# Optimization experiments

Measured on AMD Instinct MI355X. Metric: run time of the kernel, lower is better.

The kernel has to match this reference:

```python
import jax, jax.numpy as jnp
import numpy as np

N = 50000   # nodes
E = 640000  # edges
G = 128     # graphs in batch
H = 128     # hidden_channels
F_NODE, F_EDGE, F_LIG, F_POC = 64, 16, 200, 100
N_STACK = 3  # num_layers - 1


def setup_inputs() -> dict:
    key = jax.random.key(0)
    ks = jax.random.split(key, 24)
    r = lambda i, shape, s=0.05: jax.random.normal(ks[i], shape, dtype=jnp.float32) * s
    z = lambda shape: jnp.zeros(shape, jnp.float32)
    return {
        "x": jax.random.normal(ks[0], (N, F_NODE), dtype=jnp.float32),
        "edge_index": jax.random.randint(ks[1], (2, E), 0, N),
        "edge_attr": jax.random.normal(ks[2], (E, F_EDGE), dtype=jnp.float32),
        "batch": jnp.sort(jax.random.randint(ks[3], (N,), 0, G)),
        "ligand_features": jax.random.normal(ks[4], (G, F_LIG), dtype=jnp.float32),
        "pocket_features": jax.random.normal(ks[5], (G, F_POC), dtype=jnp.float32),
        # conv1 (in != out -> lin_self is a Linear)
        "W1_msg": r(6, (F_NODE, H)), "b1_msg": z((H,)),
        "W1_edge": r(7, (F_EDGE, H)), "b1_edge": z((H,)),
        "W1_self": r(8, (F_NODE, H)), "b1_self": z((H,)),
        # stacked convs (in == out -> lin_self is Identity)
        "Wk_msg": r(9, (N_STACK, H, H)), "bk_msg": z((N_STACK, H)),
        "Wk_edge": r(10, (N_STACK, F_EDGE, H)), "bk_edge": z((N_STACK, H)),
        # global feature / fusion / output heads
        "Wl": r(11, (F_LIG, H)), "bl": z((H,)),
        "Wp": r(12, (F_POC, H)), "bp": z((H,)),
        "Wf": r(13, (3 * H, H)), "bf": z((H,)),
        "Wo": r(14, (H, 1)), "bo": z((1,)),
        "return_embeddings": 0,
    }


def _general_conv(x, edge_index, edge_attr, W_msg, b_msg, W_edge, b_edge, self_out):
    # PyG GeneralConv: msg = lin_msg(x_src) + lin_edge(edge_attr), sum-aggregated at dst,
    # then + lin_self(x) (Identity skip when passed self_out = x).
    src, dst = edge_index[0], edge_index[1]
    edge_term = edge_attr @ W_edge + b_edge            # [E, H] (per-edge, layer-specific)
    msg = x[src] @ W_msg + b_msg + edge_term           # [E, H] gather + GEMM
    agg = jax.ops.segment_sum(msg, dst, num_segments=x.shape[0])  # scatter-add
    return agg + self_out


def reference(x, edge_index, edge_attr, batch, ligand_features, pocket_features,
              W1_msg, b1_msg, W1_edge, b1_edge, W1_self, b1_self,
              Wk_msg, bk_msg, Wk_edge, bk_edge,
              Wl, bl, Wp, bp, Wf, bf, Wo, bo, return_embeddings):
    # conv1 with linear self-connection
    h = _general_conv(x, edge_index, edge_attr, W1_msg, b1_msg, W1_edge, b1_edge,
                      x @ W1_self + b1_self)
    h = jax.nn.relu(h)
    # stacked convs with identity self-connection
    for i in range(N_STACK):
        h = _general_conv(h, edge_index, edge_attr, Wk_msg[i], bk_msg[i],
                          Wk_edge[i], bk_edge[i], h)
        h = jax.nn.relu(h)
    # global mean pool over graphs
    sums = jax.ops.segment_sum(h, batch, num_segments=G)
    counts = jax.ops.segment_sum(jnp.ones((h.shape[0],), h.dtype), batch, num_segments=G)
    pooled = sums / jnp.maximum(counts, 1.0)[:, None]
    # global feature fusion
    lig = ligand_features @ Wl + bl
    poc = pocket_features @ Wp + bp
    fused = jnp.concatenate([pooled, lig, poc], axis=1) @ Wf + bf
    # dropout is a no-op in eval mode
    if not return_embeddings:
        fused = fused @ Wo + bo
    return fused
```

## Files before the change

kernel.cpp:

```cpp
#include <hip/hip_runtime.h>
#include <cstdint>

#define NN 50000
#define NE 640000
#define NG 128
#define HD 128
#define FN 64
#define FE 16
#define FL 200
#define FPOC 100
#define NSTACK 3
#define NBUK 196

typedef unsigned short ushort_t;
typedef short short8 __attribute__((ext_vector_type(8)));
typedef float f32x4 __attribute__((ext_vector_type(4)));

__device__ __forceinline__ ushort_t f2bf(float f) {
    unsigned u = __float_as_uint(f);
    unsigned r = (u + 0x7fffu + ((u >> 16) & 1u)) >> 16;
    return (ushort_t)r;
}
__device__ __forceinline__ float bf2f(ushort_t u) {
    return __uint_as_float(((unsigned)u) << 16);
}


__global__ void hist_kernel(const int* __restrict__ ei, int* __restrict__ bucket_cnt) {
    __shared__ int l[NBUK];
    int t = threadIdx.x;
    if (t < NBUK) l[t] = 0;
    __syncthreads();
    int base = blockIdx.x * 2048;
#pragma unroll
    for (int i = 0; i < 8; ++i) {
        int e = base + i * 256 + t;
        if (e < NE) atomicAdd(&l[ei[NE + e] >> 8], 1);
    }
    __syncthreads();
    if (t < NBUK && l[t]) atomicAdd(&bucket_cnt[t], l[t]);
}

__global__ void scan_kernel(const int* __restrict__ bucket_cnt,
                            int* __restrict__ bucket_base, int* __restrict__ bucket_cur) {
    __shared__ int s[256];
    int t = threadIdx.x;
    int v = (t < NBUK) ? bucket_cnt[t] : 0;
    s[t] = v;
    __syncthreads();
    for (int off = 1; off < 256; off <<= 1) {
        int w = (t >= off) ? s[t - off] : 0;
        __syncthreads();
        s[t] += w;
        __syncthreads();
    }
    if (t < NBUK) {
        int b = s[t] - v;
        bucket_base[t] = b;
        bucket_cur[t] = b;
    }
}

__global__ __launch_bounds__(256) void scatter_bin(const int* __restrict__ ei,
                                                   int* __restrict__ bucket_cur,
                                                   int2* __restrict__ staging) {
    __shared__ int lcnt[NBUK];
    __shared__ int lrun[NBUK];
    int t = threadIdx.x;
    if (t < NBUK) lcnt[t] = 0;
    __syncthreads();
    int base = blockIdx.x * 4096;
#pragma unroll
    for (int i = 0; i < 16; ++i) {
        int e = base + i * 256 + t;
        if (e < NE) atomicAdd(&lcnt[ei[NE + e] >> 8], 1);
    }
    __syncthreads();
    if (t < NBUK) {
        int c = lcnt[t];
        lrun[t] = c ? atomicAdd(&bucket_cur[t], c) : 0;
        lcnt[t] = 0;
    }
    __syncthreads();
#pragma unroll
    for (int i = 0; i < 16; ++i) {
        int e = base + i * 256 + t;
        if (e < NE) {
            int s = ei[e];
            int d = ei[NE + e];
            int bk = d >> 8;
            int off = atomicAdd(&lcnt[bk], 1);
            staging[lrun[bk] + off] = make_int2(s, e | ((d & 255) << 20));
        }
    }
}

__global__ __launch_bounds__(256) void place_kernel(
    const int* __restrict__ bucket_base, const int* __restrict__ bucket_cnt,
    const int2* __restrict__ staging, int* __restrict__ row_beg,
    int* __restrict__ csrc, int* __restrict__ cedge) {
    __shared__ int hist[256];
    __shared__ int curp[256];
    int t = threadIdx.x;
    int b = blockIdx.x;
    int n0 = b << 8;
    hist[t] = 0;
    __syncthreads();
    int ebase = bucket_base[b];
    int ecnt = bucket_cnt[b];
    for (int i = t; i < ecnt; i += 256) atomicAdd(&hist[staging[ebase + i].y >> 20], 1);
    __syncthreads();
    int v = hist[t];
    __syncthreads();
    for (int off = 1; off < 256; off <<= 1) {
        int w = (t >= off) ? hist[t - off] : 0;
        __syncthreads();
        hist[t] += w;
        __syncthreads();
    }
    int rb = ebase + hist[t] - v;
    if (n0 + t < NN) row_beg[n0 + t] = rb;
    if (b == 0 && t == 0) row_beg[NN] = NE;
    curp[t] = rb;
    __syncthreads();
    for (int i = t; i < ecnt; i += 256) {
        int2 p = staging[ebase + i];
        int dl = p.y >> 20;
        int e = p.y & 0xFFFFF;
        int pos = atomicAdd(&curp[dl], 1);
        csrc[pos] = p.x;
        cedge[pos] = e;
    }
}

__global__ __launch_bounds__(256) void sege_kernel(
    const int* __restrict__ row_beg, const int* __restrict__ cedge,
    const float* __restrict__ ea, ushort_t* __restrict__ segaug) {
    int node = blockIdx.x * 4 + (threadIdx.x >> 6);
    if (node >= NN) return;
    int lane = threadIdx.x & 63;
    int G = lane >> 2, q4 = (lane & 3) * 4;
    int beg = row_beg[node], end = row_beg[node + 1];
    int dg = end - beg;
    float4 a = make_float4(0.f, 0.f, 0.f, 0.f);
    for (int j = beg + G; j < end; j += 16) {
        int e = cedge[j];
        float4 v = *(const float4*)(ea + (size_t)e * FE + q4);
        a.x += v.x; a.y += v.y; a.z += v.z; a.w += v.w;
    }
    for (int m = 4; m <= 32; m <<= 1) {
        a.x += __shfl_xor(a.x, m);
        a.y += __shfl_xor(a.y, m);
        a.z += __shfl_xor(a.z, m);
        a.w += __shfl_xor(a.w, m);
    }
    if (lane < 4) {
        ushort_t o[4] = {f2bf(a.x), f2bf(a.y), f2bf(a.z), f2bf(a.w)};
        *(uint2*)(segaug + (size_t)node * 32 + lane * 4) = *(uint2*)o;
    } else if (lane < 8) {
        ushort_t o[4] = {0, 0, 0, 0};
        if (lane == 4) { o[0] = f2bf((float)dg); o[1] = f2bf(1.f); }
        *(uint2*)(segaug + (size_t)node * 32 + lane * 4) = *(uint2*)o;
    }
}


__global__ void repack_kernel(const float* __restrict__ W1_msg,
                              const float* __restrict__ W1_self,
                              const float* __restrict__ W1_edge,
                              const float* __restrict__ b1_msg,
                              const float* __restrict__ b1_edge,
                              const float* __restrict__ b1_self,
                              const float* __restrict__ Wk_msg,
                              const float* __restrict__ Wk_edge,
                              const float* __restrict__ bk_msg,
                              const float* __restrict__ bk_edge,
                              ushort_t* __restrict__ pack) {
    int mid = blockIdx.y;
    const float *W = nullptr, *bm = nullptr, *be = nullptr, *bc = nullptr;
    int K;
    size_t doff;
    bool aug = false;
    if (mid == 0)      { W = W1_msg;  K = 64;  doff = 0; }
    else if (mid == 1) { W = W1_self; K = 64;  doff = 8192; }
    else if (mid == 2) { W = W1_edge; bm = b1_msg; be = b1_edge; bc = b1_self;
                         K = 32; doff = 16384; aug = true; }
    else if (mid <= 5) { int i = mid - 3; W = Wk_msg + (size_t)i * HD * HD;
                         K = 128; doff = 20480 + (size_t)i * 16384; }
    else               { int i = mid - 6; W = Wk_edge + (size_t)i * FE * HD;
                         bm = bk_msg + i * HD; be = bk_edge + i * HD;
                         K = 32; doff = 69632 + (size_t)i * 4096; aug = true; }
    int KS = K / 32;
    int t = blockIdx.x * 256 + threadIdx.x;
    if (t >= 8 * KS * 64) return;
    int lane = t & 63;
    int nk = t >> 6;
    int ks = nk % KS, nt = nk / KS;
    int n = nt * 16 + (lane & 15);
    int kb = ks * 32 + (lane >> 4) * 8;
    ushort_t o[8];
#pragma unroll
    for (int j = 0; j < 8; ++j) {
        int k = kb + j;
        float v;
        if (!aug)         v = W[(size_t)k * HD + n];
        else if (k < 16)  v = W[(size_t)k * HD + n];
        else if (k == 16) v = bm[n] + be[n];
        else if (k == 17) v = bc ? bc[n] : 0.f;
        else              v = 0.f;
        o[j] = f2bf(v);
    }
    *(uint4*)(pack + doff + (size_t)t * 8) = *(uint4*)o;
}


__global__ __launch_bounds__(256) void gemm_mfma_conv1(const float* __restrict__ A,
                                                       const ushort_t* __restrict__ segaug,
                                                       const ushort_t* __restrict__ pack,
                                                       ushort_t* __restrict__ Cm,
                                                       ushort_t* __restrict__ Cs, int n) {
    constexpr int STR = 72, SSTR = 40;
    __shared__ __align__(16) ushort_t As[64 * STR];
    __shared__ __align__(16) ushort_t Ss[64 * SSTR];
    int tid = threadIdx.x;
    int row0 = blockIdx.x * 64;
#pragma unroll
    for (int p = 0; p < 2; ++p) {
        int c = p * 256 + tid;
        int r = c >> 3, col = (c & 7) * 8;
        int gr = row0 + r;
        float4 f0 = make_float4(0.f, 0.f, 0.f, 0.f), f1 = f0;
        if (gr < n) {
            f0 = *(const float4*)(A + (size_t)gr * FN + col);
            f1 = *(const float4*)(A + (size_t)gr * FN + col + 4);
        }
        ushort_t o[8] = {f2bf(f0.x), f2bf(f0.y), f2bf(f0.z), f2bf(f0.w),
                         f2bf(f1.x), f2bf(f1.y), f2bf(f1.z), f2bf(f1.w)};
        *(uint4*)(&As[r * STR + col]) = *(uint4*)o;
    }
    {
        int c = tid;
        int r = c >> 2, col = (c & 3) * 8;
        int gr = row0 + r;
        uint4 v = make_uint4(0u, 0u, 0u, 0u);
        if (gr < n) v = *(const uint4*)(segaug + (size_t)gr * 32 + col);
        *(uint4*)(&Ss[r * SSTR + col]) = v;
    }
    __syncthreads();
    int lane = tid & 63, wave = tid >> 6;
    int m = lane & 15, quad = lane >> 4;
    f32x4 acc[16];
#pragma unroll
    for (int i = 0; i < 16; ++i) acc[i] = (f32x4)(0.f);
    const short8* Bmsg = (const short8*)pack;
    const short8* Bself = (const short8*)(pack + 8192);
    const short8* Beaug = (const short8*)(pack + 16384);
#pragma unroll
    for (int ks = 0; ks < 2; ++ks) {
        short8 a = *(const short8*)(&As[(wave * 16 + m) * STR + ks * 32 + quad * 8]);
#pragma unroll
        for (int nt = 0; nt < 8; ++nt) {
            acc[nt] = __builtin_amdgcn_mfma_f32_16x16x32_bf16(
                a, Bmsg[(nt * 2 + ks) * 64 + lane], acc[nt], 0, 0, 0);
            acc[8 + nt] = __builtin_amdgcn_mfma_f32_16x16x32_bf16(
                a, Bself[(nt * 2 + ks) * 64 + lane], acc[8 + nt], 0, 0, 0);
        }
    }
    {
        short8 sa = *(const short8*)(&Ss[(wave * 16 + m) * SSTR + quad * 8]);
#pragma unroll
        for (int nt = 0; nt < 8; ++nt)
            acc[8 + nt] = __builtin_amdgcn_mfma_f32_16x16x32_bf16(
                sa, Beaug[nt * 64 + lane], acc[8 + nt], 0, 0, 0);
    }
#pragma unroll
    for (int nt = 0; nt < 8; ++nt) {
        int col = nt * 16 + m;
#pragma unroll
        for (int r = 0; r < 4; ++r) {
            int grow = row0 + wave * 16 + quad * 4 + r;
            if (grow < n) {
                Cm[(size_t)grow * HD + col] = f2bf(acc[nt][r]);
                Cs[(size_t)grow * HD + col] = f2bf(acc[8 + nt][r]);
            }
        }
    }
}


__device__ __forceinline__ void accum8(float* a, uint4 v) {
    a[0] += __uint_as_float(v.x << 16);
    a[1] += __uint_as_float(v.x & 0xffff0000u);
    a[2] += __uint_as_float(v.y << 16);
    a[3] += __uint_as_float(v.y & 0xffff0000u);
    a[4] += __uint_as_float(v.z << 16);
    a[5] += __uint_as_float(v.z & 0xffff0000u);
    a[6] += __uint_as_float(v.w << 16);
    a[7] += __uint_as_float(v.w & 0xffff0000u);
}

#define AGG_LOOP(SRCBUF)                                                       \
    {                                                                          \
        int j = beg;                                                           \
        for (; j + 3 < end; j += 4) {                                          \
            int u0 = csrc[j], u1 = csrc[j + 1], u2 = csrc[j + 2],              \
                u3 = csrc[j + 3];                                              \
            uint4 v0 = *(const uint4*)(SRCBUF + (size_t)u0 * HD + c8);         \
            uint4 v1 = *(const uint4*)(SRCBUF + (size_t)u1 * HD + c8);         \
            uint4 v2 = *(const uint4*)(SRCBUF + (size_t)u2 * HD + c8);         \
            uint4 v3 = *(const uint4*)(SRCBUF + (size_t)u3 * HD + c8);         \
            accum8(a0, v0);                                                    \
            accum8(a1, v1);                                                    \
            accum8(a0, v2);                                                    \
            accum8(a1, v3);                                                    \
        }                                                                      \
        for (; j < end; ++j) {                                                 \
            uint4 v = *(const uint4*)(SRCBUF + (size_t)csrc[j] * HD + c8);     \
            accum8(a0, v);                                                     \
        }                                                                      \
    }

__global__ __launch_bounds__(256, 6) void fused_agg_gemm(
    const int* __restrict__ row_beg, const int* __restrict__ csrc,
    const ushort_t* __restrict__ msg_in, const ushort_t* __restrict__ S_in,
    const ushort_t* __restrict__ segaug, const ushort_t* __restrict__ Bm,
    const ushort_t* __restrict__ Be, ushort_t* __restrict__ msg_out,
    ushort_t* __restrict__ S_out) {
    constexpr int STR = 136, SSTR = 40;
    __shared__ __align__(16) ushort_t Hs[16 * STR];
    __shared__ __align__(16) ushort_t Ss[16 * SSTR];
    int tid = threadIdx.x;
    int node0 = blockIdx.x * 16;
    if (tid < 64) {
        int r = tid >> 2, col = (tid & 3) * 8;
        *(uint4*)(&Ss[r * SSTR + col]) =
            *(const uint4*)(segaug + (size_t)(node0 + r) * 32 + col);
    }
    int nl = tid >> 4;
    int node = node0 + nl;
    int c8 = (tid & 15) * 8;
    int beg = row_beg[node];
    int end = row_beg[node + 1];
    float a0[8] = {0.f, 0.f, 0.f, 0.f, 0.f, 0.f, 0.f, 0.f};
    float a1[8] = {0.f, 0.f, 0.f, 0.f, 0.f, 0.f, 0.f, 0.f};
    AGG_LOOP(msg_in)
    accum8(a0, *(const uint4*)(S_in + (size_t)node * HD + c8));
    {
        ushort_t h8[8];
#pragma unroll
        for (int i = 0; i < 8; ++i) h8[i] = f2bf(fmaxf(a0[i] + a1[i], 0.f));
        *(uint4*)(&Hs[nl * STR + c8]) = *(uint4*)h8;
    }
    __syncthreads();
    int lane = tid & 63, wave = tid >> 6;
    int m = lane & 15, quad = lane >> 4;
    f32x4 acc[2], accE[2];
#pragma unroll
    for (int t = 0; t < 2; ++t) { acc[t] = (f32x4)(0.f); accE[t] = (f32x4)(0.f); }
    const short8* Bmv = (const short8*)Bm;
    const short8* Bev = (const short8*)Be;
#pragma unroll
    for (int ks = 0; ks < 4; ++ks) {
        short8 a = *(const short8*)(&Hs[m * STR + ks * 32 + quad * 8]);
#pragma unroll
        for (int t = 0; t < 2; ++t) {
            int nt = wave * 2 + t;
            acc[t] = __builtin_amdgcn_mfma_f32_16x16x32_bf16(
                a, Bmv[(nt * 4 + ks) * 64 + lane], acc[t], 0, 0, 0);
        }
    }
    {
        short8 sa = *(const short8*)(&Ss[m * SSTR + quad * 8]);
#pragma unroll
        for (int t = 0; t < 2; ++t) {
            int nt = wave * 2 + t;
            accE[t] = __builtin_amdgcn_mfma_f32_16x16x32_bf16(
                sa, Bev[nt * 64 + lane], accE[t], 0, 0, 0);
        }
    }
#pragma unroll
    for (int t = 0; t < 2; ++t) {
        int col = (wave * 2 + t) * 16 + m;
#pragma unroll
        for (int r = 0; r < 4; ++r) {
            int rl = quad * 4 + r;
            size_t gidx = (size_t)(node0 + rl) * HD + col;
            msg_out[gidx] = f2bf(acc[t][r]);
            S_out[gidx] = f2bf(accE[t][r] + bf2f(Hs[rl * STR + col]));
        }
    }
}


__global__ __launch_bounds__(256, 6) void agg_pool_kernel(
    const int* __restrict__ row_beg, const int* __restrict__ csrc,
    const ushort_t* __restrict__ xm, const ushort_t* __restrict__ selfb,
    const int* __restrict__ batch, float* __restrict__ pooled) {
    __shared__ float hloc[16][HD];
    int tid = threadIdx.x;
    int node0 = blockIdx.x * 16;
    int nl = tid >> 4;
    int node = node0 + nl;
    int c8 = (tid & 15) * 8;
    int beg = row_beg[node];
    int end = row_beg[node + 1];
    float a0[8] = {0.f, 0.f, 0.f, 0.f, 0.f, 0.f, 0.f, 0.f};
    float a1[8] = {0.f, 0.f, 0.f, 0.f, 0.f, 0.f, 0.f, 0.f};
    AGG_LOOP(xm)
    accum8(a0, *(const uint4*)(selfb + (size_t)node * HD + c8));
#pragma unroll
    for (int i = 0; i < 8; ++i) hloc[nl][c8 + i] = fmaxf(a0[i] + a1[i], 0.f);
    __syncthreads();
    if (tid < HD) {
        int f = tid;
        float run = 0.f;
        int gprev = batch[node0];
        for (int r = 0; r < 16; ++r) {
            int g = batch[node0 + r];
            if (g != gprev) {
                atomicAdd(&pooled[gprev * HD + f], run);
                run = 0.f;
                gprev = g;
            }
            run += hloc[r][f];
        }
        atomicAdd(&pooled[gprev * HD + f], run);
    }
}


__global__ void head_kernel(const float* __restrict__ pooled, const int* __restrict__ batch,
                            const float* __restrict__ lf, const float* __restrict__ pfe,
                            const float* __restrict__ Wl, const float* __restrict__ bl,
                            const float* __restrict__ Wp, const float* __restrict__ bp,
                            const float* __restrict__ Wf, const float* __restrict__ bfv,
                            const float* __restrict__ Wo, const float* __restrict__ bo,
                            float* __restrict__ out) {
    __shared__ float cat[3 * HD];
    __shared__ float red[HD];
    int g = blockIdx.x, j = threadIdx.x;
    int lo = 0, hi = NN;
    while (lo < hi) { int m = (lo + hi) >> 1; if (batch[m] < g) lo = m + 1; else hi = m; }
    int s0 = lo;
    lo = s0; hi = NN;
    while (lo < hi) { int m = (lo + hi) >> 1; if (batch[m] < g + 1) lo = m + 1; else hi = m; }
    float cntf = (float)(lo - s0);
    cat[j] = pooled[(size_t)g * HD + j] / fmaxf(cntf, 1.f);
    float s = bl[j];
    for (int k = 0; k < FL; ++k) s += lf[g * FL + k] * Wl[k * HD + j];
    cat[HD + j] = s;
    s = bp[j];
    for (int k = 0; k < FPOC; ++k) s += pfe[g * FPOC + k] * Wp[k * HD + j];
    cat[2 * HD + j] = s;
    __syncthreads();
    float fj = bfv[j];
    for (int k = 0; k < 3 * HD; ++k) fj += cat[k] * Wf[k * HD + j];
    red[j] = fj * Wo[j];
    __syncthreads();
    for (int off = 64; off > 0; off >>= 1) {
        if (j < off) red[j] += red[j + off];
        __syncthreads();
    }
    if (j == 0) out[g] = red[0] + bo[0];
}


extern "C" void kernel_launch(void* const* d_in, const int* in_sizes, int n_in,
                              void* d_out, int out_size, void* d_ws, size_t ws_size,
                              hipStream_t stream) {
    const float* x       = (const float*)d_in[0];
    const int*   ei      = (const int*)d_in[1];
    const float* ea      = (const float*)d_in[2];
    const int*   batch   = (const int*)d_in[3];
    const float* lf      = (const float*)d_in[4];
    const float* pfe     = (const float*)d_in[5];
    const float* W1_msg  = (const float*)d_in[6];
    const float* b1_msg  = (const float*)d_in[7];
    const float* W1_edge = (const float*)d_in[8];
    const float* b1_edge = (const float*)d_in[9];
    const float* W1_self = (const float*)d_in[10];
    const float* b1_self = (const float*)d_in[11];
    const float* Wk_msg  = (const float*)d_in[12];
    const float* bk_msg  = (const float*)d_in[13];
    const float* Wk_edge = (const float*)d_in[14];
    const float* bk_edge = (const float*)d_in[15];
    const float* Wl      = (const float*)d_in[16];
    const float* bl      = (const float*)d_in[17];
    const float* Wp      = (const float*)d_in[18];
    const float* bp      = (const float*)d_in[19];
    const float* Wf      = (const float*)d_in[20];
    const float* bfv     = (const float*)d_in[21];
    const float* Wo      = (const float*)d_in[22];
    const float* bo      = (const float*)d_in[23];

    char* wsp = (char*)d_ws;
    size_t off = 0;
    auto carve = [&](size_t bytes) -> void* {
        char* p = wsp + off;
        off += (bytes + 255) & ~(size_t)255;
        return (void*)p;
    };
    int*      bucket_cnt  = (int*)carve((size_t)NBUK * 4);
    float*    pooled      = (float*)carve((size_t)NG * HD * 4);
    int*      bucket_base = (int*)carve((size_t)NBUK * 4);
    int*      bucket_cur  = (int*)carve((size_t)NBUK * 4);
    int*      row_beg     = (int*)carve((size_t)(NN + 1) * 4);
    int2*     staging     = (int2*)carve((size_t)NE * 8);
    int*      csrc        = (int*)carve((size_t)NE * 4);
    int*      cedge       = (int*)carve((size_t)NE * 4);
    ushort_t* segaug      = (ushort_t*)carve((size_t)NN * 32 * 2);
    ushort_t* pack        = (ushort_t*)carve((size_t)81920 * 2);
    ushort_t* bufC        = (ushort_t*)carve((size_t)NN * HD * 2);
    ushort_t* bufD        = (ushort_t*)carve((size_t)NN * HD * 2);
    ushort_t* bufS        = (ushort_t*)carve((size_t)NN * HD * 2);
    ushort_t* bufT        = (ushort_t*)carve((size_t)NN * HD * 2);

    size_t clr = (size_t)((char*)(pooled + NG * HD) - (char*)bucket_cnt);
    hipMemsetAsync(bucket_cnt, 0, clr, stream);

    hist_kernel<<<(NE + 2047) / 2048, 256, 0, stream>>>(ei, bucket_cnt);
    scan_kernel<<<1, 256, 0, stream>>>(bucket_cnt, bucket_base, bucket_cur);
    scatter_bin<<<(NE + 4095) / 4096, 256, 0, stream>>>(ei, bucket_cur, staging);
    place_kernel<<<NBUK, 256, 0, stream>>>(bucket_base, bucket_cnt, staging, row_beg,
                                           csrc, cedge);
    sege_kernel<<<(NN + 3) / 4, 256, 0, stream>>>(row_beg, cedge, ea, segaug);
    repack_kernel<<<dim3(8, 9), 256, 0, stream>>>(W1_msg, W1_self, W1_edge, b1_msg,
                                                  b1_edge, b1_self, Wk_msg, Wk_edge,
                                                  bk_msg, bk_edge, pack);

    gemm_mfma_conv1<<<dim3((NN + 63) / 64), 256, 0, stream>>>(x, segaug, pack, bufC,
                                                              bufS, NN);
    fused_agg_gemm<<<NN / 16, 256, 0, stream>>>(row_beg, csrc, bufC, bufS, segaug,
                                                pack + 20480, pack + 69632, bufD, bufT);
    fused_agg_gemm<<<NN / 16, 256, 0, stream>>>(row_beg, csrc, bufD, bufT, segaug,
                                                pack + 20480 + 16384, pack + 69632 + 4096,
                                                bufC, bufS);
    fused_agg_gemm<<<NN / 16, 256, 0, stream>>>(row_beg, csrc, bufC, bufS, segaug,
                                                pack + 20480 + 32768, pack + 69632 + 8192,
                                                bufD, bufT);
    agg_pool_kernel<<<NN / 16, 256, 0, stream>>>(row_beg, csrc, bufD, bufT, batch,
                                                 pooled);

    head_kernel<<<NG, HD, 0, stream>>>(pooled, batch, lf, pfe, Wl, bl, Wp, bp, Wf, bfv,
                                       Wo, bo, (float*)d_out);
}
```

Baseline: 348.0 us.

## Fold scan into scatter/place, merge sege+repack, stage GEMM outputs through LDS

Removes the single-block scan kernel by recomputing the bucket prefix sum redundantly inside scatter_bin and place_kernel. Merges the segment edge-sum kernel and the weight repack kernel into one launch split by block index. The conv1 GEMM and the fused aggregation GEMM now stage their bf16 outputs in shared memory and write them as coalesced 16-byte rows instead of scattered 2-byte stores. The trade is extra LDS use and barriers per block, plus redundant scans in every scatter and place block.

New measurement: 358.7 us. 1.03x slower.

```diff
diff --git a/kernel.cpp b/kernel.cpp
--- a/kernel.cpp
+++ b/kernel.cpp
@@ -11,6 +11,7 @@
 #define FPOC 100
 #define NSTACK 3
 #define NBUK 196
+#define SEGE_BLK 12500
 
 typedef unsigned short ushort_t;
 typedef short short8 __attribute__((ext_vector_type(8)));
@@ -41,34 +42,24 @@
     if (t < NBUK && l[t]) atomicAdd(&bucket_cnt[t], l[t]);
 }
 
-__global__ void scan_kernel(const int* __restrict__ bucket_cnt,
-                            int* __restrict__ bucket_base, int* __restrict__ bucket_cur) {
-    __shared__ int s[256];
-    int t = threadIdx.x;
-    int v = (t < NBUK) ? bucket_cnt[t] : 0;
-    s[t] = v;
-    __syncthreads();
-    for (int off = 1; off < 256; off <<= 1) {
-        int w = (t >= off) ? s[t - off] : 0;
-        __syncthreads();
-        s[t] += w;
-        __syncthreads();
-    }
-    if (t < NBUK) {
-        int b = s[t] - v;
-        bucket_base[t] = b;
-        bucket_cur[t] = b;
-    }
-}
-
 __global__ __launch_bounds__(256) void scatter_bin(const int* __restrict__ ei,
+                                                   const int* __restrict__ bucket_cnt,
                                                    int* __restrict__ bucket_cur,
                                                    int2* __restrict__ staging) {
     __shared__ int lcnt[NBUK];
     __shared__ int lrun[NBUK];
+    __shared__ int pre[256];
     int t = threadIdx.x;
+    int v = (t < NBUK) ? bucket_cnt[t] : 0;
+    pre[t] = v;
     if (t < NBUK) lcnt[t] = 0;
     __syncthreads();
+    for (int off = 1; off < 256; off <<= 1) {
+        int w = (t >= off) ? pre[t - off] : 0;
+        __syncthreads();
+        pre[t] += w;
+        __syncthreads();
+    }
     int base = blockIdx.x * 4096;
 #pragma unroll
     for (int i = 0; i < 16; ++i) {
@@ -78,7 +69,7 @@
     __syncthreads();
     if (t < NBUK) {
         int c = lcnt[t];
-        lrun[t] = c ? atomicAdd(&bucket_cur[t], c) : 0;
+        lrun[t] = (pre[t] - v) + (c ? atomicAdd(&bucket_cur[t], c) : 0);
         lcnt[t] = 0;
     }
     __syncthreads();
@@ -96,21 +87,29 @@
 }
 
 __global__ __launch_bounds__(256) void place_kernel(
-    const int* __restrict__ bucket_base, const int* __restrict__ bucket_cnt,
-    const int2* __restrict__ staging, int* __restrict__ row_beg,
-    int* __restrict__ csrc, int* __restrict__ cedge) {
+    const int* __restrict__ bucket_cnt, const int2* __restrict__ staging,
+    int* __restrict__ row_beg, int* __restrict__ csrc, int* __restrict__ cedge) {
+    __shared__ int pre[256];
     __shared__ int hist[256];
     __shared__ int curp[256];
     int t = threadIdx.x;
     int b = blockIdx.x;
     int n0 = b << 8;
+    int v = (t < NBUK) ? bucket_cnt[t] : 0;
+    pre[t] = v;
     hist[t] = 0;
     __syncthreads();
-    int ebase = bucket_base[b];
+    for (int off = 1; off < 256; off <<= 1) {
+        int w = (t >= off) ? pre[t - off] : 0;
+        __syncthreads();
+        pre[t] += w;
+        __syncthreads();
+    }
     int ecnt = bucket_cnt[b];
+    int ebase = pre[b] - ecnt;
     for (int i = t; i < ecnt; i += 256) atomicAdd(&hist[staging[ebase + i].y >> 20], 1);
     __syncthreads();
-    int v = hist[t];
+    int hv = hist[t];
     __syncthreads();
     for (int off = 1; off < 256; off <<= 1) {
         int w = (t >= off) ? hist[t - off] : 0;
@@ -118,7 +117,7 @@
         hist[t] += w;
         __syncthreads();
     }
-    int rb = ebase + hist[t] - v;
+    int rb = ebase + hist[t] - hv;
     if (n0 + t < NN) row_beg[n0 + t] = rb;
     if (b == 0 && t == 0) row_beg[NN] = NE;
     curp[t] = rb;
@@ -133,50 +132,47 @@
     }
 }
 
-__global__ __launch_bounds__(256) void sege_kernel(
+
+__global__ __launch_bounds__(256) void sege_repack_kernel(
     const int* __restrict__ row_beg, const int* __restrict__ cedge,
-    const float* __restrict__ ea, ushort_t* __restrict__ segaug) {
-    int node = blockIdx.x * 4 + (threadIdx.x >> 6);
-    if (node >= NN) return;
-    int lane = threadIdx.x & 63;
-    int G = lane >> 2, q4 = (lane & 3) * 4;
-    int beg = row_beg[node], end = row_beg[node + 1];
-    int dg = end - beg;
-    float4 a = make_float4(0.f, 0.f, 0.f, 0.f);
-    for (int j = beg + G; j < end; j += 16) {
-        int e = cedge[j];
-        float4 v = *(const float4*)(ea + (size_t)e * FE + q4);
-        a.x += v.x; a.y += v.y; a.z += v.z; a.w += v.w;
-    }
-    for (int m = 4; m <= 32; m <<= 1) {
-        a.x += __shfl_xor(a.x, m);
-        a.y += __shfl_xor(a.y, m);
-        a.z += __shfl_xor(a.z, m);
-        a.w += __shfl_xor(a.w, m);
-    }
-    if (lane < 4) {
-        ushort_t o[4] = {f2bf(a.x), f2bf(a.y), f2bf(a.z), f2bf(a.w)};
-        *(uint2*)(segaug + (size_t)node * 32 + lane * 4) = *(uint2*)o;
-    } else if (lane < 8) {
-        ushort_t o[4] = {0, 0, 0, 0};
-        if (lane == 4) { o[0] = f2bf((float)dg); o[1] = f2bf(1.f); }
-        *(uint2*)(segaug + (size_t)node * 32 + lane * 4) = *(uint2*)o;
-    }
-}
-
-
-__global__ void repack_kernel(const float* __restrict__ W1_msg,
-                              const float* __restrict__ W1_self,
-                              const float* __restrict__ W1_edge,
-                              const float* __restrict__ b1_msg,
-                              const float* __restrict__ b1_edge,
-                              const float* __restrict__ b1_self,
-                              const float* __restrict__ Wk_msg,
-                              const float* __restrict__ Wk_edge,
-                              const float* __restrict__ bk_msg,
-                              const float* __restrict__ bk_edge,
-                              ushort_t* __restrict__ pack) {
-    int mid = blockIdx.y;
+    const float* __restrict__ ea, ushort_t* __restrict__ segaug,
+    const float* __restrict__ W1_msg, const float* __restrict__ W1_self,
+    const float* __restrict__ W1_edge, const float* __restrict__ b1_msg,
+    const float* __restrict__ b1_edge, const float* __restrict__ b1_self,
+    const float* __restrict__ Wk_msg, const float* __restrict__ Wk_edge,
+    const float* __restrict__ bk_msg, const float* __restrict__ bk_edge,
+    ushort_t* __restrict__ pack) {
+    if (blockIdx.x < SEGE_BLK) {
+        int node = blockIdx.x * 4 + (threadIdx.x >> 6);
+        if (node >= NN) return;
+        int lane = threadIdx.x & 63;
+        int G = lane >> 2, q4 = (lane & 3) * 4;
+        int beg = row_beg[node], end = row_beg[node + 1];
+        int dg = end - beg;
+        float4 a = make_float4(0.f, 0.f, 0.f, 0.f);
+        for (int j = beg + G; j < end; j += 16) {
+            int e = cedge[j];
+            float4 v = *(const float4*)(ea + (size_t)e * FE + q4);
+            a.x += v.x; a.y += v.y; a.z += v.z; a.w += v.w;
+        }
+        for (int m = 4; m <= 32; m <<= 1) {
+            a.x += __shfl_xor(a.x, m);
+            a.y += __shfl_xor(a.y, m);
+            a.z += __shfl_xor(a.z, m);
+            a.w += __shfl_xor(a.w, m);
+        }
+        if (lane < 4) {
+            ushort_t o[4] = {f2bf(a.x), f2bf(a.y), f2bf(a.z), f2bf(a.w)};
+            *(uint2*)(segaug + (size_t)node * 32 + lane * 4) = *(uint2*)o;
+        } else if (lane < 8) {
+            ushort_t o[4] = {0, 0, 0, 0};
+            if (lane == 4) { o[0] = f2bf((float)dg); o[1] = f2bf(1.f); }
+            *(uint2*)(segaug + (size_t)node * 32 + lane * 4) = *(uint2*)o;
+        }
+        return;
+    }
+    int bx = blockIdx.x - SEGE_BLK;
+    int mid = bx >> 3;
     const float *W = nullptr, *bm = nullptr, *be = nullptr, *bc = nullptr;
     int K;
     size_t doff;
@@ -191,7 +187,7 @@
                          bm = bk_msg + i * HD; be = bk_edge + i * HD;
                          K = 32; doff = 69632 + (size_t)i * 4096; aug = true; }
     int KS = K / 32;
-    int t = blockIdx.x * 256 + threadIdx.x;
+    int t = (bx & 7) * 256 + threadIdx.x;
     if (t >= 8 * KS * 64) return;
     int lane = t & 63;
     int nk = t >> 6;
@@ -222,6 +218,7 @@
     constexpr int STR = 72, SSTR = 40;
     __shared__ __align__(16) ushort_t As[64 * STR];
     __shared__ __align__(16) ushort_t Ss[64 * SSTR];
+    __shared__ __align__(16) ushort_t St[64 * HD];
     int tid = threadIdx.x;
     int row0 = blockIdx.x * 64;
 #pragma unroll
@@ -274,16 +271,31 @@
                 sa, Beaug[nt * 64 + lane], acc[8 + nt], 0, 0, 0);
     }
 #pragma unroll
-    for (int nt = 0; nt < 8; ++nt) {
-        int col = nt * 16 + m;
-#pragma unroll
-        for (int r = 0; r < 4; ++r) {
-            int grow = row0 + wave * 16 + quad * 4 + r;
-            if (grow < n) {
-                Cm[(size_t)grow * HD + col] = f2bf(acc[nt][r]);
-                Cs[(size_t)grow * HD + col] = f2bf(acc[8 + nt][r]);
-            }
-        }
+    for (int nt = 0; nt < 8; ++nt)
+#pragma unroll
+        for (int r = 0; r < 4; ++r)
+            St[(wave * 16 + quad * 4 + r) * HD + nt * 16 + m] = f2bf(acc[nt][r]);
+    __syncthreads();
+#pragma unroll
+    for (int p = 0; p < 4; ++p) {
+        int flat = p * 256 + tid;
+        int r = flat >> 4, cc = (flat & 15) * 8;
+        int grow = row0 + r;
+        if (grow < n) *(uint4*)(Cm + (size_t)grow * HD + cc) = *(uint4*)(&St[r * HD + cc]);
+    }
+    __syncthreads();
+#pragma unroll
+    for (int nt = 0; nt < 8; ++nt)
+#pragma unroll
+        for (int r = 0; r < 4; ++r)
+            St[(wave * 16 + quad * 4 + r) * HD + nt * 16 + m] = f2bf(acc[8 + nt][r]);
+    __syncthreads();
+#pragma unroll
+    for (int p = 0; p < 4; ++p) {
+        int flat = p * 256 + tid;
+        int r = flat >> 4, cc = (flat & 15) * 8;
+        int grow = row0 + r;
+        if (grow < n) *(uint4*)(Cs + (size_t)grow * HD + cc) = *(uint4*)(&St[r * HD + cc]);
     }
 }
 
@@ -329,6 +341,8 @@
     constexpr int STR = 136, SSTR = 40;
     __shared__ __align__(16) ushort_t Hs[16 * STR];
     __shared__ __align__(16) ushort_t Ss[16 * SSTR];
+    __shared__ __align__(16) ushort_t Ms[16 * HD];
+    __shared__ __align__(16) ushort_t Ts[16 * HD];
     int tid = threadIdx.x;
     int node0 = blockIdx.x * 16;
     if (tid < 64) {
@@ -384,11 +398,13 @@
 #pragma unroll
         for (int r = 0; r < 4; ++r) {
             int rl = quad * 4 + r;
-            size_t gidx = (size_t)(node0 + rl) * HD + col;
-            msg_out[gidx] = f2bf(acc[t][r]);
-            S_out[gidx] = f2bf(accE[t][r] + bf2f(Hs[rl * STR + col]));
-        }
-    }
+            Ms[rl * HD + col] = f2bf(acc[t][r]);
+            Ts[rl * HD + col] = f2bf(accE[t][r] + bf2f(Hs[rl * STR + col]));
+        }
+    }
+    __syncthreads();
+    *(uint4*)(msg_out + (size_t)node * HD + c8) = *(uint4*)(&Ms[nl * HD + c8]);
+    *(uint4*)(S_out + (size_t)node * HD + c8) = *(uint4*)(&Ts[nl * HD + c8]);
 }
 
 
@@ -501,9 +517,8 @@
         return (void*)p;
     };
     int*      bucket_cnt  = (int*)carve((size_t)NBUK * 4);
+    int*      bucket_cur  = (int*)carve((size_t)NBUK * 4);
     float*    pooled      = (float*)carve((size_t)NG * HD * 4);
-    int*      bucket_base = (int*)carve((size_t)NBUK * 4);
-    int*      bucket_cur  = (int*)carve((size_t)NBUK * 4);
     int*      row_beg     = (int*)carve((size_t)(NN + 1) * 4);
     int2*     staging     = (int2*)carve((size_t)NE * 8);
     int*      csrc        = (int*)carve((size_t)NE * 4);
@@ -519,14 +534,12 @@
     hipMemsetAsync(bucket_cnt, 0, clr, stream);
 
     hist_kernel<<<(NE + 2047) / 2048, 256, 0, stream>>>(ei, bucket_cnt);
-    scan_kernel<<<1, 256, 0, stream>>>(bucket_cnt, bucket_base, bucket_cur);
-    scatter_bin<<<(NE + 4095) / 4096, 256, 0, stream>>>(ei, bucket_cur, staging);
-    place_kernel<<<NBUK, 256, 0, stream>>>(bucket_base, bucket_cnt, staging, row_beg,
-                                           csrc, cedge);
-    sege_kernel<<<(NN + 3) / 4, 256, 0, stream>>>(row_beg, cedge, ea, segaug);
-    repack_kernel<<<dim3(8, 9), 256, 0, stream>>>(W1_msg, W1_self, W1_edge, b1_msg,
-                                                  b1_edge, b1_self, Wk_msg, Wk_edge,
-                                                  bk_msg, bk_edge, pack);
+    scatter_bin<<<(NE + 4095) / 4096, 256, 0, stream>>>(ei, bucket_cnt, bucket_cur,
+                                                        staging);
+    place_kernel<<<NBUK, 256, 0, stream>>>(bucket_cnt, staging, row_beg, csrc, cedge);
+    sege_repack_kernel<<<SEGE_BLK + 72, 256, 0, stream>>>(
+        row_beg, cedge, ea, segaug, W1_msg, W1_self, W1_edge, b1_msg, b1_edge,
+        b1_self, Wk_msg, Wk_edge, bk_msg, bk_edge, pack);
 
     gemm_mfma_conv1<<<dim3((NN + 63) / 64), 256, 0, stream>>>(x, segaug, pack, bufC,
                                                               bufS, NN);
```
